# Optimization experiments

Hardware: AMD Instinct MI355X
Metric: run time of the kernel (lower is better)

## Reference

```python
import jax, jax.numpy as jnp
import numpy as np

H = 8  # n_heads

def setup_inputs() -> dict:
    key = jax.random.key(0)
    k1, k2, k3, k4, k5 = jax.random.split(key, 5)
    B, N, D = 4, 2048, 512
    x = jax.random.normal(k1, (B, N, D), dtype=jnp.float32)
    mask_flat = jax.random.randint(k2, (B, N), 0, 2).astype(bool)
    s = 1.0 / np.sqrt(D)
    Wq = jax.random.normal(k3, (D, D), dtype=jnp.float32) * s
    Wkv = jax.random.normal(k4, (D, 2 * D), dtype=jnp.float32) * s
    Wo = jax.random.normal(k5, (D, D), dtype=jnp.float32) * s
    return {"x": x, "mask_flat": mask_flat, "Wq": Wq, "Wkv": Wkv, "Wo": Wo}

def reference(x, mask_flat, Wq, Wkv, Wo):
    B, N, D = x.shape
    d = D // H
    scale = d ** -0.5
    kv = x @ Wkv                                   # (B,N,2D)
    k, v = jnp.split(kv, 2, axis=-1)
    q = x @ Wq                                     # (B,N,D)
    # (B,H,N,d)
    q = q.reshape(B, N, H, d).transpose(0, 2, 1, 3)
    k = k.reshape(B, N, H, d).transpose(0, 2, 1, 3)
    v = v.reshape(B, N, H, d).transpose(0, 2, 1, 3)
    attn = jax.nn.softmax(jnp.einsum('bhmd,bhnd->bhmn', q, k) * scale, axis=-1)
    res = jnp.einsum('bhmn,bhnd->bhmd', attn, v)   # (B,H,N,d)
    out = res.transpose(0, 2, 1, 3).reshape(B, N, D) @ Wo
    # non-masked query positions produce zero output (residual elsewhere keeps them)
    return jnp.where(mask_flat[..., None], out, 0.0)
```

## Files before the change

### kernel.cpp

```cpp
#include <hip/hip_runtime.h>

typedef __bf16 bf16x8 __attribute__((ext_vector_type(8)));
typedef float f32x4 __attribute__((ext_vector_type(4)));
typedef float f32x16 __attribute__((ext_vector_type(16)));
typedef unsigned short u16x8 __attribute__((ext_vector_type(8)));
typedef unsigned int u32x4 __attribute__((ext_vector_type(4)));
typedef int i32x2 __attribute__((ext_vector_type(2)));

__device__ inline unsigned short f2bf(float f) {
    __bf16 h = (__bf16)f;
    return __builtin_bit_cast(unsigned short, h);
}

__device__ inline unsigned int pkbf(float lo, float hi) {
    return (unsigned int)f2bf(lo) | ((unsigned int)f2bf(hi) << 16);
}

__device__ inline float fexp2(float x) {
#if __has_builtin(__builtin_amdgcn_exp2f)
    return __builtin_amdgcn_exp2f(x);
#else
    return exp2f(x);
#endif
}

__device__ inline f32x4 mfma16(u16x8 a, u16x8 b, f32x4 c) {
    return __builtin_amdgcn_mfma_f32_16x16x32_bf16(
        __builtin_bit_cast(bf16x8, a), __builtin_bit_cast(bf16x8, b), c, 0, 0, 0);
}

__device__ inline f32x16 mfma32(u16x8 a, u16x8 b, f32x16 c) {
    return __builtin_amdgcn_mfma_f32_32x32x16_bf16(
        __builtin_bit_cast(bf16x8, a), __builtin_bit_cast(bf16x8, b), c, 0, 0, 0);
}

__device__ inline i32x2 permswap(unsigned int a, unsigned int b, int hi) {
#if __has_builtin(__builtin_amdgcn_permlane32_swap)
    (void)hi;
    return __builtin_amdgcn_permlane32_swap((int)a, (int)b, false, false);
#else
    int pa_ = __shfl_xor((int)a, 32);
    int pb_ = __shfl_xor((int)b, 32);
    i32x2 r;
    r[0] = hi ? pb_ : (int)a;
    r[1] = hi ? (int)b : pa_;
    return r;
#endif
}

__device__ inline void gld_lds16(const unsigned short* gsrc, unsigned short* ldst) {
    __builtin_amdgcn_global_load_lds(
        (const __attribute__((address_space(1))) unsigned int*)gsrc,
        (__attribute__((address_space(3))) unsigned int*)ldst, 16, 0, 0);
}

#define WAIT_VM(n)                                          \
    asm volatile("s_waitcnt vmcnt(" #n ")" ::: "memory");   \
    __builtin_amdgcn_sched_barrier(0)
#define WAIT_LGKM0                                          \
    asm volatile("s_waitcnt lgkmcnt(0)" ::: "memory");      \
    __builtin_amdgcn_sched_barrier(0)
#define BARRIER                                             \
    __builtin_amdgcn_s_barrier();                           \
    __builtin_amdgcn_sched_barrier(0)

__global__ __launch_bounds__(256) void cvt_f32_bf16(const float* __restrict__ in,
                                                    unsigned short* __restrict__ out, long n) {
    long i = ((long)blockIdx.x * blockDim.x + threadIdx.x) * 4;
    if (i >= n) return;
    float4 v = *(const float4*)(in + i);
    ushort4 r;
    r.x = f2bf(v.x); r.y = f2bf(v.y); r.z = f2bf(v.z); r.w = f2bf(v.w);
    *(ushort4*)(out + i) = r;
}

__global__ __launch_bounds__(256) void transpose_cvt_tiled(const float* __restrict__ W,
                                                           unsigned short* __restrict__ Wt,
                                                           int K, int N, float scale) {
    __shared__ float tile[64][65];
    const int n0 = blockIdx.x * 64, k0 = blockIdx.y * 64;
    const int c = threadIdx.x & 63;
    const int r4 = threadIdx.x >> 6;
#pragma unroll
    for (int i = 0; i < 16; i++) {
        int r = r4 * 16 + i;
        tile[r][c] = W[(long)(k0 + r) * N + n0 + c];
    }
    __syncthreads();
#pragma unroll
    for (int i = 0; i < 16; i++) {
        int rr = r4 * 16 + i;
        Wt[(long)(n0 + rr) * K + k0 + c] = f2bf(tile[c][rr] * scale);
    }
}

template<int WRITE_BF16, int MASKED>
__global__ __launch_bounds__(256) void gemm_bt(const unsigned short* __restrict__ A,
                                               const unsigned short* __restrict__ Bt,
                                               void* __restrict__ Cv,
                                               int M, int N, int K,
                                               const int* __restrict__ mask) {
    __shared__ unsigned short AsL[2][128 * 32];
    __shared__ unsigned short BsL[2][128 * 32];
    const int tid = threadIdx.x;
    const int lane = tid & 63;
    const int wid = tid >> 6;
    const int lg = lane >> 4, lr = lane & 15;
    const int wm = wid >> 1, wn = wid & 1;
    const long m0 = (long)blockIdx.y * 128, n0 = (long)blockIdx.x * 128;

    f32x4 acc[4][4] = {};

    const unsigned short* aS0 = A  + (m0 + (tid >> 2)) * K + (tid & 3) * 8;
    const unsigned short* aS1 = A  + (m0 + 64 + (tid >> 2)) * K + (tid & 3) * 8;
    const unsigned short* bS0 = Bt + (n0 + (tid >> 2)) * K + (tid & 3) * 8;
    const unsigned short* bS1 = Bt + (n0 + 64 + (tid >> 2)) * K + (tid & 3) * 8;

#define GSTAGE(bufi, k0v)                                    \
    {                                                        \
        gld_lds16(aS0 + (k0v), &AsL[bufi][wid * 512]);       \
        gld_lds16(aS1 + (k0v), &AsL[bufi][2048 + wid * 512]);\
        gld_lds16(bS0 + (k0v), &BsL[bufi][wid * 512]);       \
        gld_lds16(bS1 + (k0v), &BsL[bufi][2048 + wid * 512]);\
    }

#define GREAD(cur)                                                                    \
    {                                                                                 \
        _Pragma("unroll")                                                             \
        for (int i = 0; i < 4; i++) {                                                 \
            af[i]  = *(const u16x8*)&AsL[cur][(wm * 64 + i * 16 + lr) * 32 + lg * 8]; \
            bfr[i] = *(const u16x8*)&BsL[cur][(wn * 64 + i * 16 + lr) * 32 + lg * 8]; \
        }                                                                             \
    }

#define GMFMA                                                                  \
    {                                                                          \
        _Pragma("unroll")                                                      \
        for (int i = 0; i < 4; i++)                                            \
            _Pragma("unroll")                                                  \
            for (int j = 0; j < 4; j++)                                        \
                acc[i][j] = mfma16(af[i], bfr[j], acc[i][j]);                  \
    }

    const int nk = K >> 5;
    GSTAGE(0, 0);
    GSTAGE(1, 32);
    for (int t = 0; t < nk - 1; t++) {
        const int cur = t & 1;
        u16x8 af[4], bfr[4];
        WAIT_VM(4);
        BARRIER;
        GREAD(cur);
        WAIT_LGKM0;
        BARRIER;
        if (t < nk - 2) GSTAGE(cur, (t + 2) * 32);
        GMFMA;
    }
    {
        u16x8 af[4], bfr[4];
        WAIT_VM(0);
        BARRIER;
        GREAD((nk - 1) & 1);
        GMFMA;
    }
#undef GSTAGE
#undef GREAD
#undef GMFMA

#pragma unroll
    for (int i = 0; i < 4; i++)
#pragma unroll
        for (int j = 0; j < 4; j++)
#pragma unroll
            for (int r = 0; r < 4; r++) {
                long row = m0 + wm * 64 + i * 16 + lg * 4 + r;
                long col = n0 + wn * 64 + j * 16 + lr;
                float v = acc[i][j][r];
                if (MASKED) {
                    if (!mask[row]) v = 0.0f;
                    ((float*)Cv)[row * N + col] = v;
                } else if (WRITE_BF16) {
                    ((unsigned short*)Cv)[row * N + col] = f2bf(v);
                } else {
                    ((float*)Cv)[row * N + col] = v;
                }
            }
}

__global__ __launch_bounds__(256) void attn_kernel(const unsigned short* __restrict__ qk,
                                                   const unsigned short* __restrict__ vT,
                                                   unsigned short* __restrict__ res) {
    const int Nseq = 2048, LD = 1024;
    const long T = 8192;
    const int id = blockIdx.x;
    const int xcd = id & 7, jj = id >> 3;
    const int g = xcd + 8 * (jj & 3);
    const int qt = jj >> 2;
    const int b = g >> 3, h = g & 7;

    const int tid = threadIdx.x;
    const int wid = tid >> 6, lane = tid & 63;
    const int qL = lane & 31, hi = lane >> 5;

    __shared__ unsigned short KsL[2][4096];
    __shared__ unsigned short VsL[2][4096];

    const int qbase = qt * 128 + wid * 32;
    const long qrow = (long)b * Nseq + qbase + qL;
    u16x8 qf[4];
#pragma unroll
    for (int j = 0; j < 4; j++)
        qf[j] = *(const u16x8*)(qk + qrow * LD + h * 64 + 16 * j + 8 * hi);

    f32x16 oacc[2] = {};
    f32x16 lacc = {};
    u16x8 onesf;
#pragma unroll
    for (int e = 0; e < 8; e++) onesf[e] = 0x3F80;

    const int Rsub = lane >> 3, psw = ((lane & 7) ^ (Rsub & 7)) * 8;
    const int R0 = 16 * wid + Rsub;
    const unsigned short* kS = qk + 512 + ((long)b * Nseq + R0) * LD + h * 64 + psw;
    const unsigned short* vS = vT + ((long)h * 64 + R0) * T + (long)b * Nseq + psw;
    const int rsw = qL & 7;

#define STAGE(bufi)                                                            \
    {                                                                          \
        gld_lds16(kS,             &KsL[bufi][(2 * wid + 0) * 512]);            \
        gld_lds16(kS + 8L * LD,   &KsL[bufi][(2 * wid + 1) * 512]);            \
        gld_lds16(vS,             &VsL[bufi][(2 * wid + 0) * 512]);            \
        gld_lds16(vS + 8L * T,    &VsL[bufi][(2 * wid + 1) * 512]);            \
        kS += 64L * LD; vS += 64;                                              \
    }

#define READ_KF(buf)                                                           \
    {                                                                          \
        _Pragma("unroll")                                                      \
        for (int kvb = 0; kvb < 2; kvb++)                                      \
            _Pragma("unroll")                                                  \
            for (int j = 0; j < 4; j++)                                        \
                kf[kvb][j] = *(const u16x8*)&KsL[buf][(kvb * 32 + qL) * 64     \
                                                      + ((2 * j + hi) ^ rsw) * 8]; \
    }
#define READ_VF(buf)                                                           \
    {                                                                          \
        _Pragma("unroll")                                                      \
        for (int db = 0; db < 2; db++)                                         \
            _Pragma("unroll")                                                  \
            for (int jk = 0; jk < 4; jk++)                                     \
                vf[db][jk] = *(const u16x8*)&VsL[buf][(db * 32 + qL) * 64      \
                                                      + ((2 * jk + hi) ^ rsw) * 8]; \
    }

#define PACK_PV(SC)                                                                    \
    {                                                                                  \
        u16x8 pa[4];                                                                   \
        _Pragma("unroll")                                                              \
        for (int kvb = 0; kvb < 2; kvb++) {                                            \
            unsigned int w[8];                                                         \
            _Pragma("unroll")                                                          \
            for (int i = 0; i < 8; i++)                                                \
                w[i] = pkbf(fexp2(SC[kvb][2 * i]), fexp2(SC[kvb][2 * i + 1]));         \
            _Pragma("unroll")                                                          \
            for (int hh = 0; hh < 2; hh++) {                                           \
                i32x2 ra = permswap(w[4 * hh + 0], w[4 * hh + 2], hi);                 \
                i32x2 rb = permswap(w[4 * hh + 1], w[4 * hh + 3], hi);                 \
                u32x4 fw;                                                              \
                fw[0] = (unsigned)ra[0]; fw[1] = (unsigned)rb[0];                      \
                fw[2] = (unsigned)ra[1]; fw[3] = (unsigned)rb[1];                      \
                pa[kvb * 2 + hh] = __builtin_bit_cast(u16x8, fw);                      \
            }                                                                          \
        }                                                                              \
        _Pragma("unroll")                                                              \
        for (int jk = 0; jk < 4; jk++) {                                               \
            lacc = mfma32(pa[jk], onesf, lacc);                                        \
            oacc[0] = mfma32(pa[jk], vf[0][jk], oacc[0]);                              \
            oacc[1] = mfma32(pa[jk], vf[1][jk], oacc[1]);                              \
        }                                                                              \
    }

#define QKNEXT(SN)                                                                     \
    {                                                                                  \
        SN[0] = (f32x16){}; SN[1] = (f32x16){};                                        \
        _Pragma("unroll")                                                              \
        for (int j = 0; j < 4; j++) {                                                  \
            SN[0] = mfma32(kf[0][j], qf[j], SN[0]);                                    \
            SN[1] = mfma32(kf[1][j], qf[j], SN[1]);                                    \
        }                                                                              \
    }

#define STEP(SC, SN, rdbufK, rdbufV, doStage, stagebuf)                                \
    {                                                                                  \
        WAIT_VM(2);                                                                    \
        BARRIER;                                                                       \
        READ_KF(rdbufK);                                                               \
        READ_VF(rdbufV);                                                               \
        WAIT_LGKM0;                                                                    \
        BARRIER;                                                                       \
        if (doStage) STAGE(stagebuf);                                                  \
        QKNEXT(SN);                                                                    \
        PACK_PV(SC);                                                                   \
    }

    u16x8 kf[2][4], vf[2][4];
    f32x16 sA2[2], sB2[2];

    STAGE(0);
    STAGE(1);
    WAIT_VM(6);
    BARRIER;
    READ_KF(0);
    WAIT_LGKM0;
    QKNEXT(sA2);

    for (int t = 0; t < 30; t += 2) {
        STEP(sA2, sB2, 1, 0, 1, 0);
        STEP(sB2, sA2, 0, 1, 1, 1);
    }
    {
        WAIT_VM(2);
        BARRIER;
        READ_KF(1);
        READ_VF(0);
        WAIT_LGKM0;
        QKNEXT(sB2);
        PACK_PV(sA2);
    }
    {
        WAIT_VM(0);
        BARRIER;
        READ_VF(1);
        WAIT_LGKM0;
        PACK_PV(sB2);
    }
#undef STAGE
#undef READ_KF
#undef READ_VF
#undef PACK_PV
#undef QKNEXT
#undef STEP

#pragma unroll
    for (int reg = 0; reg < 16; reg++) {
        const int crow = (reg & 3) + 8 * (reg >> 2) + 4 * hi;
        float linv = 1.0f / lacc[reg];
        long row = (long)b * Nseq + qbase + crow;
        res[row * 512 + h * 64 + qL]      = f2bf(oacc[0][reg] * linv);
        res[row * 512 + h * 64 + 32 + qL] = f2bf(oacc[1][reg] * linv);
    }
}

extern "C" void kernel_launch(void* const* d_in, const int* in_sizes, int n_in,
                              void* d_out, int out_size, void* d_ws, size_t ws_size,
                              hipStream_t stream) {
    const float* x   = (const float*)d_in[0];
    const int* mask  = (const int*)d_in[1];
    const float* Wq  = (const float*)d_in[2];
    const float* Wkv = (const float*)d_in[3];
    const float* Wo  = (const float*)d_in[4];
    float* out = (float*)d_out;

    const int Nseq = 2048, D = 512;
    const long T = 8192;
    const float QSCALE = 0.125f * 1.4426950408889634f;

    unsigned short* ws    = (unsigned short*)d_ws;
    unsigned short* xb    = ws;
    unsigned short* WqkvT = xb    + T * D;
    unsigned short* WoT   = WqkvT + 1536L * 512;
    unsigned short* qkb   = WoT   + 512L * 512;
    unsigned short* vTb   = qkb   + T * 1024;
    unsigned short* resb  = vTb   + 512L * T;

    cvt_f32_bf16<<<(int)(T * D / 1024), 256, 0, stream>>>(x, xb, T * D);
    transpose_cvt_tiled<<<dim3(8, 8),  256, 0, stream>>>(Wq,  WqkvT,              D, 512,  QSCALE);
    transpose_cvt_tiled<<<dim3(16, 8), 256, 0, stream>>>(Wkv, WqkvT + 512L * 512, D, 1024, 1.0f);
    transpose_cvt_tiled<<<dim3(8, 8),  256, 0, stream>>>(Wo,  WoT,                D, 512,  1.0f);

    gemm_bt<1, 0><<<dim3(8, 64), 256, 0, stream>>>(xb, WqkvT, qkb, T, 1024, D, nullptr);
    gemm_bt<1, 0><<<dim3(64, 4), 256, 0, stream>>>(WqkvT + 1024L * 512, xb, vTb, D, T, D, nullptr);

    attn_kernel<<<512, 256, 0, stream>>>(qkb, vTb, resb);

    gemm_bt<0, 1><<<dim3(4, 64), 256, 0, stream>>>(resb, WoT, out, T, D, D, mask);
}
```

Measured before the change: 105.7 us.

## Compact masked query rows to skip attention and output projection work

Adds a per-batch prefix scan over the mask that builds a compacted list of active query indices. The attention kernel then processes only active queries, using 64-query blocks of 128 threads with a deeper staging count, and writes compacted results. The output projection runs on the compacted rows and scatters them to their original positions, while a separate kernel zeroes the masked rows. This removes roughly half the attention and Wo work for a random mask, at the cost of extra launches, gather/scatter indexing and smaller attention blocks.

```diff
diff --git a/kernel.cpp b/kernel.cpp
--- a/kernel.cpp
+++ b/kernel.cpp
@@ -94,12 +94,41 @@
     }
 }
 
-template<int WRITE_BF16, int MASKED>
+__global__ __launch_bounds__(256) void scan_mask(const int* __restrict__ mask,
+                                                 int* __restrict__ idx, int* __restrict__ cnt) {
+    const int b = blockIdx.x;
+    const int tid = threadIdx.x;
+    __shared__ int wsum[4];
+    int m[8]; int pc = 0;
+#pragma unroll
+    for (int k = 0; k < 8; k++) { m[k] = mask[b * 2048 + tid * 8 + k]; pc += (m[k] != 0); }
+    int s = pc;
+    const int lane = tid & 63;
+    for (int off = 1; off < 64; off <<= 1) {
+        int v = __shfl_up(s, off);
+        if (lane >= off) s += v;
+    }
+    if (lane == 63) wsum[tid >> 6] = s;
+    __syncthreads();
+    int wbase = 0;
+    for (int w = 0; w < (tid >> 6); w++) wbase += wsum[w];
+    int run = wbase + s - pc;
+#pragma unroll
+    for (int k = 0; k < 8; k++) if (m[k]) idx[b * 2048 + (run++)] = tid * 8 + k;
+    if (tid == 255) cnt[b] = wbase + s;
+}
+
+__global__ __launch_bounds__(256) void zero_masked(const int* __restrict__ mask,
+                                                   float* __restrict__ out) {
+    long gid = (long)blockIdx.x * 256 + threadIdx.x;
+    int row = (int)(gid >> 7);
+    if (!mask[row]) *(float4*)(out + gid * 4) = make_float4(0.f, 0.f, 0.f, 0.f);
+}
+
 __global__ __launch_bounds__(256) void gemm_bt(const unsigned short* __restrict__ A,
                                                const unsigned short* __restrict__ Bt,
-                                               void* __restrict__ Cv,
-                                               int M, int N, int K,
-                                               const int* __restrict__ mask) {
+                                               unsigned short* __restrict__ C,
+                                               int M, int N, int K) {
     __shared__ unsigned short AsL[2][128 * 32];
     __shared__ unsigned short BsL[2][128 * 32];
     const int tid = threadIdx.x;
@@ -123,7 +152,6 @@
         gld_lds16(bS0 + (k0v), &BsL[bufi][wid * 512]);       \
         gld_lds16(bS1 + (k0v), &BsL[bufi][2048 + wid * 512]);\
     }
-
 #define GREAD(cur)                                                                    \
     {                                                                                 \
         _Pragma("unroll")                                                             \
@@ -132,7 +160,6 @@
             bfr[i] = *(const u16x8*)&BsL[cur][(wn * 64 + i * 16 + lr) * 32 + lg * 8]; \
         }                                                                             \
     }
-
 #define GMFMA                                                                  \
     {                                                                          \
         _Pragma("unroll")                                                      \
@@ -175,21 +202,107 @@
             for (int r = 0; r < 4; r++) {
                 long row = m0 + wm * 64 + i * 16 + lg * 4 + r;
                 long col = n0 + wn * 64 + j * 16 + lr;
-                float v = acc[i][j][r];
-                if (MASKED) {
-                    if (!mask[row]) v = 0.0f;
-                    ((float*)Cv)[row * N + col] = v;
-                } else if (WRITE_BF16) {
-                    ((unsigned short*)Cv)[row * N + col] = f2bf(v);
-                } else {
-                    ((float*)Cv)[row * N + col] = v;
+                C[row * N + col] = f2bf(acc[i][j][r]);
+            }
+}
+
+__global__ __launch_bounds__(256) void gemm_scatter(const unsigned short* __restrict__ A,
+                                                    const unsigned short* __restrict__ Bt,
+                                                    float* __restrict__ out,
+                                                    int N, int K,
+                                                    const int* __restrict__ idxm,
+                                                    const int* __restrict__ cntm) {
+    const long m0 = (long)blockIdx.y * 128;
+    const int bb = (int)(m0 >> 11);
+    const int cnt = cntm[bb];
+    const int i0 = (int)(m0 & 2047);
+    if (i0 >= cnt) return;
+
+    __shared__ unsigned short AsL[2][128 * 32];
+    __shared__ unsigned short BsL[2][128 * 32];
+    const int tid = threadIdx.x;
+    const int lane = tid & 63;
+    const int wid = tid >> 6;
+    const int lg = lane >> 4, lr = lane & 15;
+    const int wm = wid >> 1, wn = wid & 1;
+    const long n0 = (long)blockIdx.x * 128;
+
+    f32x4 acc[4][4] = {};
+
+    const unsigned short* aS0 = A  + (m0 + (tid >> 2)) * K + (tid & 3) * 8;
+    const unsigned short* aS1 = A  + (m0 + 64 + (tid >> 2)) * K + (tid & 3) * 8;
+    const unsigned short* bS0 = Bt + (n0 + (tid >> 2)) * K + (tid & 3) * 8;
+    const unsigned short* bS1 = Bt + (n0 + 64 + (tid >> 2)) * K + (tid & 3) * 8;
+
+#define GSTAGE(bufi, k0v)                                    \
+    {                                                        \
+        gld_lds16(aS0 + (k0v), &AsL[bufi][wid * 512]);       \
+        gld_lds16(aS1 + (k0v), &AsL[bufi][2048 + wid * 512]);\
+        gld_lds16(bS0 + (k0v), &BsL[bufi][wid * 512]);       \
+        gld_lds16(bS1 + (k0v), &BsL[bufi][2048 + wid * 512]);\
+    }
+#define GREAD(cur)                                                                    \
+    {                                                                                 \
+        _Pragma("unroll")                                                             \
+        for (int i = 0; i < 4; i++) {                                                 \
+            af[i]  = *(const u16x8*)&AsL[cur][(wm * 64 + i * 16 + lr) * 32 + lg * 8]; \
+            bfr[i] = *(const u16x8*)&BsL[cur][(wn * 64 + i * 16 + lr) * 32 + lg * 8]; \
+        }                                                                             \
+    }
+#define GMFMA                                                                  \
+    {                                                                          \
+        _Pragma("unroll")                                                      \
+        for (int i = 0; i < 4; i++)                                            \
+            _Pragma("unroll")                                                  \
+            for (int j = 0; j < 4; j++)                                        \
+                acc[i][j] = mfma16(af[i], bfr[j], acc[i][j]);                  \
+    }
+
+    const int nk = K >> 5;
+    GSTAGE(0, 0);
+    GSTAGE(1, 32);
+    for (int t = 0; t < nk - 1; t++) {
+        const int cur = t & 1;
+        u16x8 af[4], bfr[4];
+        WAIT_VM(4);
+        BARRIER;
+        GREAD(cur);
+        WAIT_LGKM0;
+        BARRIER;
+        if (t < nk - 2) GSTAGE(cur, (t + 2) * 32);
+        GMFMA;
+    }
+    {
+        u16x8 af[4], bfr[4];
+        WAIT_VM(0);
+        BARRIER;
+        GREAD((nk - 1) & 1);
+        GMFMA;
+    }
+#undef GSTAGE
+#undef GREAD
+#undef GMFMA
+
+#pragma unroll
+    for (int i = 0; i < 4; i++)
+#pragma unroll
+        for (int j = 0; j < 4; j++)
+#pragma unroll
+            for (int r = 0; r < 4; r++) {
+                int row_c = i0 + wm * 64 + i * 16 + lg * 4 + r;
+                if (row_c < cnt) {
+                    int orig = idxm[bb * 2048 + row_c];
+                    long col = n0 + wn * 64 + j * 16 + lr;
+                    out[((long)bb * 2048 + orig) * N + col] = acc[i][j][r];
                 }
             }
 }
 
-__global__ __launch_bounds__(256) void attn_kernel(const unsigned short* __restrict__ qk,
+__global__ __launch_bounds__(128) void attn_kernel(const unsigned short* __restrict__ qk,
                                                    const unsigned short* __restrict__ vT,
-                                                   unsigned short* __restrict__ res) {
+                                                   unsigned short* __restrict__ res,
+                                                   const int* __restrict__ idxm,
+                                                   const int* __restrict__ cntm) {
     const int Nseq = 2048, LD = 1024;
     const long T = 8192;
     const int id = blockIdx.x;
@@ -198,6 +311,9 @@
     const int qt = jj >> 2;
     const int b = g >> 3, h = g & 7;
 
+    const int count = cntm[b];
+    if (qt * 64 >= count) return;
+
     const int tid = threadIdx.x;
     const int wid = tid >> 6, lane = tid & 63;
     const int qL = lane & 31, hi = lane >> 5;
@@ -205,8 +321,10 @@
     __shared__ unsigned short KsL[2][4096];
     __shared__ unsigned short VsL[2][4096];
 
-    const int qbase = qt * 128 + wid * 32;
-    const long qrow = (long)b * Nseq + qbase + qL;
+    const int qbase = qt * 64 + wid * 32;
+    const int i_q = qbase + qL;
+    const int gi = idxm[b * 2048 + (i_q < count ? i_q : count - 1)];
+    const long qrow = (long)b * Nseq + gi;
     u16x8 qf[4];
 #pragma unroll
     for (int j = 0; j < 4; j++)
@@ -219,17 +337,19 @@
     for (int e = 0; e < 8; e++) onesf[e] = 0x3F80;
 
     const int Rsub = lane >> 3, psw = ((lane & 7) ^ (Rsub & 7)) * 8;
-    const int R0 = 16 * wid + Rsub;
+    const int R0 = 32 * wid + Rsub;
     const unsigned short* kS = qk + 512 + ((long)b * Nseq + R0) * LD + h * 64 + psw;
     const unsigned short* vS = vT + ((long)h * 64 + R0) * T + (long)b * Nseq + psw;
     const int rsw = qL & 7;
 
 #define STAGE(bufi)                                                            \
     {                                                                          \
-        gld_lds16(kS,             &KsL[bufi][(2 * wid + 0) * 512]);            \
-        gld_lds16(kS + 8L * LD,   &KsL[bufi][(2 * wid + 1) * 512]);            \
-        gld_lds16(vS,             &VsL[bufi][(2 * wid + 0) * 512]);            \
-        gld_lds16(vS + 8L * T,    &VsL[bufi][(2 * wid + 1) * 512]);            \
+        _Pragma("unroll")                                                      \
+        for (int i = 0; i < 4; i++)                                            \
+            gld_lds16(kS + (long)i * 8 * LD, &KsL[bufi][(4 * wid + i) * 512]); \
+        _Pragma("unroll")                                                      \
+        for (int i = 0; i < 4; i++)                                            \
+            gld_lds16(vS + (long)i * 8 * T,  &VsL[bufi][(4 * wid + i) * 512]); \
         kS += 64L * LD; vS += 64;                                              \
     }
 
@@ -291,7 +411,7 @@
 
 #define STEP(SC, SN, rdbufK, rdbufV, doStage, stagebuf)                                \
     {                                                                                  \
-        WAIT_VM(2);                                                                    \
+        WAIT_VM(4);                                                                    \
         BARRIER;                                                                       \
         READ_KF(rdbufK);                                                               \
         READ_VF(rdbufV);                                                               \
@@ -307,7 +427,7 @@
 
     STAGE(0);
     STAGE(1);
-    WAIT_VM(6);
+    WAIT_VM(12);
     BARRIER;
     READ_KF(0);
     WAIT_LGKM0;
@@ -318,7 +438,7 @@
         STEP(sB2, sA2, 0, 1, 1, 1);
     }
     {
-        WAIT_VM(2);
+        WAIT_VM(4);
         BARRIER;
         READ_KF(1);
         READ_VF(0);
@@ -343,10 +463,13 @@
 #pragma unroll
     for (int reg = 0; reg < 16; reg++) {
         const int crow = (reg & 3) + 8 * (reg >> 2) + 4 * hi;
-        float linv = 1.0f / lacc[reg];
-        long row = (long)b * Nseq + qbase + crow;
-        res[row * 512 + h * 64 + qL]      = f2bf(oacc[0][reg] * linv);
-        res[row * 512 + h * 64 + 32 + qL] = f2bf(oacc[1][reg] * linv);
+        const int row_c = qbase + crow;
+        if (row_c < count) {
+            float linv = 1.0f / lacc[reg];
+            long row = (long)b * Nseq + row_c;
+            res[row * 512 + h * 64 + qL]      = f2bf(oacc[0][reg] * linv);
+            res[row * 512 + h * 64 + 32 + qL] = f2bf(oacc[1][reg] * linv);
+        }
     }
 }
 
@@ -371,16 +494,20 @@
     unsigned short* qkb   = WoT   + 512L * 512;
     unsigned short* vTb   = qkb   + T * 1024;
     unsigned short* resb  = vTb   + 512L * T;
+    int* idxb = (int*)(resb + T * 512);
+    int* cntb = idxb + 4 * 2048;
 
     cvt_f32_bf16<<<(int)(T * D / 1024), 256, 0, stream>>>(x, xb, T * D);
     transpose_cvt_tiled<<<dim3(8, 8),  256, 0, stream>>>(Wq,  WqkvT,              D, 512,  QSCALE);
     transpose_cvt_tiled<<<dim3(16, 8), 256, 0, stream>>>(Wkv, WqkvT + 512L * 512, D, 1024, 1.0f);
     transpose_cvt_tiled<<<dim3(8, 8),  256, 0, stream>>>(Wo,  WoT,                D, 512,  1.0f);
-
-    gemm_bt<1, 0><<<dim3(8, 64), 256, 0, stream>>>(xb, WqkvT, qkb, T, 1024, D, nullptr);
-    gemm_bt<1, 0><<<dim3(64, 4), 256, 0, stream>>>(WqkvT + 1024L * 512, xb, vTb, D, T, D, nullptr);
-
-    attn_kernel<<<512, 256, 0, stream>>>(qkb, vTb, resb);
-
-    gemm_bt<0, 1><<<dim3(4, 64), 256, 0, stream>>>(resb, WoT, out, T, D, D, mask);
-}
+    scan_mask<<<4, 256, 0, stream>>>(mask, idxb, cntb);
+
+    gemm_bt<<<dim3(8, 64), 256, 0, stream>>>(xb, WqkvT, qkb, T, 1024, D);
+    gemm_bt<<<dim3(64, 4), 256, 0, stream>>>(WqkvT + 1024L * 512, xb, vTb, D, T, D);
+
+    attn_kernel<<<1024, 128, 0, stream>>>(qkb, vTb, resb, idxb, cntb);
+
+    zero_masked<<<(int)(T * 512 / 1024), 256, 0, stream>>>(mask, out);
+    gemm_scatter<<<dim3(4, 64), 256, 0, stream>>>(resb, WoT, out, D, D, idxb, cntb);
+}
```

Measured after the change: 115.8 us. 1.09x slower.

## Compact masked query rows and split KV range across waves in attention

Applied to the files above, without the earlier changes.

Adds a per-batch prefix-scan kernel that compacts the indices of masked-in query positions, so attention runs only over query rows whose output survives the final mask. Each block now handles 64 compacted queries, with the four waves split into two query halves times two KV halves. Each wave stages its own K/V tiles without block barriers, and the partial outputs and row sums are merged through LDS at the end. This roughly halves attention work for a random mask, at the cost of an extra launch, gathered Q loads and scattered result writes. Unmasked rows of res are left unwritten, which is safe only because the output GEMM zeros those rows.

```diff
diff --git a/kernel.cpp b/kernel.cpp
--- a/kernel.cpp
+++ b/kernel.cpp
@@ -92,6 +92,30 @@
         int rr = r4 * 16 + i;
         Wt[(long)(n0 + rr) * K + k0 + c] = f2bf(tile[c][rr] * scale);
     }
+}
+
+__global__ __launch_bounds__(256) void scan_mask(const int* __restrict__ mask,
+                                                 int* __restrict__ idx, int* __restrict__ cnt) {
+    const int b = blockIdx.x;
+    const int tid = threadIdx.x;
+    __shared__ int wsum[4];
+    int m[8]; int pc = 0;
+#pragma unroll
+    for (int k = 0; k < 8; k++) { m[k] = mask[b * 2048 + tid * 8 + k]; pc += (m[k] != 0); }
+    int s = pc;
+    const int lane = tid & 63;
+    for (int off = 1; off < 64; off <<= 1) {
+        int v = __shfl_up(s, off);
+        if (lane >= off) s += v;
+    }
+    if (lane == 63) wsum[tid >> 6] = s;
+    __syncthreads();
+    int wbase = 0;
+    for (int w = 0; w < (tid >> 6); w++) wbase += wsum[w];
+    int run = wbase + s - pc;
+#pragma unroll
+    for (int k = 0; k < 8; k++) if (m[k]) idx[b * 2048 + (run++)] = tid * 8 + k;
+    if (tid == 255) cnt[b] = wbase + s;
 }
 
 template<int WRITE_BF16, int MASKED>
@@ -123,7 +147,6 @@
         gld_lds16(bS0 + (k0v), &BsL[bufi][wid * 512]);       \
         gld_lds16(bS1 + (k0v), &BsL[bufi][2048 + wid * 512]);\
     }
-
 #define GREAD(cur)                                                                    \
     {                                                                                 \
         _Pragma("unroll")                                                             \
@@ -132,7 +155,6 @@
             bfr[i] = *(const u16x8*)&BsL[cur][(wn * 64 + i * 16 + lr) * 32 + lg * 8]; \
         }                                                                             \
     }
-
 #define GMFMA                                                                  \
     {                                                                          \
         _Pragma("unroll")                                                      \
@@ -189,7 +211,9 @@
 
 __global__ __launch_bounds__(256) void attn_kernel(const unsigned short* __restrict__ qk,
                                                    const unsigned short* __restrict__ vT,
-                                                   unsigned short* __restrict__ res) {
+                                                   unsigned short* __restrict__ res,
+                                                   const int* __restrict__ idxm,
+                                                   const int* __restrict__ cntm) {
     const int Nseq = 2048, LD = 1024;
     const long T = 8192;
     const int id = blockIdx.x;
@@ -198,15 +222,20 @@
     const int qt = jj >> 2;
     const int b = g >> 3, h = g & 7;
 
+    const int count = cntm[b];
+    if (qt * 64 >= count) return;
+
     const int tid = threadIdx.x;
     const int wid = tid >> 6, lane = tid & 63;
     const int qL = lane & 31, hi = lane >> 5;
-
-    __shared__ unsigned short KsL[2][4096];
-    __shared__ unsigned short VsL[2][4096];
-
-    const int qbase = qt * 128 + wid * 32;
-    const long qrow = (long)b * Nseq + qbase + qL;
+    const int qh = wid >> 1, kvh = wid & 1;
+
+    __shared__ unsigned short LDSB[4][2][4096];
+    unsigned short* myL = &LDSB[wid][0][0];
+
+    const int i_q = qt * 64 + qh * 32 + qL;
+    const int gi = idxm[b * 2048 + (i_q < count ? i_q : count - 1)];
+    const long qrow = (long)b * Nseq + gi;
     u16x8 qf[4];
 #pragma unroll
     for (int j = 0; j < 4; j++)
@@ -218,135 +247,151 @@
 #pragma unroll
     for (int e = 0; e < 8; e++) onesf[e] = 0x3F80;
 
-    const int Rsub = lane >> 3, psw = ((lane & 7) ^ (Rsub & 7)) * 8;
-    const int R0 = 16 * wid + Rsub;
-    const unsigned short* kS = qk + 512 + ((long)b * Nseq + R0) * LD + h * 64 + psw;
-    const unsigned short* vS = vT + ((long)h * 64 + R0) * T + (long)b * Nseq + psw;
+    const int R0 = lane >> 3, p0 = lane & 7;
+    const unsigned short* kS = qk + 512 + ((long)b * Nseq + kvh * 1024 + R0) * LD + h * 64
+                               + ((p0 ^ R0) * 8);
+    const int rV = lane >> 2, pV = lane & 3;
+    const unsigned short* vS = vT + ((long)h * 64 + rV) * T + (long)b * Nseq + kvh * 1024
+                               + ((pV ^ ((lane >> 3) & 3)) * 8);
     const int rsw = qL & 7;
 
-#define STAGE(bufi)                                                            \
-    {                                                                          \
-        gld_lds16(kS,             &KsL[bufi][(2 * wid + 0) * 512]);            \
-        gld_lds16(kS + 8L * LD,   &KsL[bufi][(2 * wid + 1) * 512]);            \
-        gld_lds16(vS,             &VsL[bufi][(2 * wid + 0) * 512]);            \
-        gld_lds16(vS + 8L * T,    &VsL[bufi][(2 * wid + 1) * 512]);            \
-        kS += 64L * LD; vS += 64;                                              \
+#define STAGE(bufi)                                                          \
+    {                                                                        \
+        unsigned short* dK = myL + (bufi) * 4096;                            \
+        _Pragma("unroll")                                                    \
+        for (int i = 0; i < 4; i++)                                          \
+            gld_lds16(kS + (long)i * 8 * LD, dK + i * 512);                  \
+        _Pragma("unroll")                                                    \
+        for (int i = 0; i < 4; i++)                                          \
+            gld_lds16(vS + (long)i * 16 * T, dK + 2048 + i * 512);           \
+        kS += 32L * LD; vS += 32;                                            \
     }
 
 #define READ_KF(buf)                                                           \
     {                                                                          \
         _Pragma("unroll")                                                      \
-        for (int kvb = 0; kvb < 2; kvb++)                                      \
-            _Pragma("unroll")                                                  \
-            for (int j = 0; j < 4; j++)                                        \
-                kf[kvb][j] = *(const u16x8*)&KsL[buf][(kvb * 32 + qL) * 64     \
-                                                      + ((2 * j + hi) ^ rsw) * 8]; \
+        for (int j = 0; j < 4; j++)                                            \
+            kf[j] = *(const u16x8*)&myL[(buf) * 4096 + qL * 64                 \
+                                        + (((2 * j + hi) ^ rsw) * 8)];         \
     }
 #define READ_VF(buf)                                                           \
     {                                                                          \
         _Pragma("unroll")                                                      \
         for (int db = 0; db < 2; db++)                                         \
             _Pragma("unroll")                                                  \
-            for (int jk = 0; jk < 4; jk++)                                     \
-                vf[db][jk] = *(const u16x8*)&VsL[buf][(db * 32 + qL) * 64      \
-                                                      + ((2 * jk + hi) ^ rsw) * 8]; \
+            for (int jk = 0; jk < 2; jk++)                                     \
+                vf[db][jk] = *(const u16x8*)&myL[(buf) * 4096 + 2048           \
+                                 + (db * 32 + qL) * 32                         \
+                                 + (((2 * jk + hi) ^ ((qL >> 1) & 3)) * 8)];   \
+    }
+
+#define QKNEXT(SN)                                                             \
+    {                                                                          \
+        SN = (f32x16){};                                                       \
+        _Pragma("unroll")                                                      \
+        for (int j = 0; j < 4; j++) SN = mfma32(kf[j], qf[j], SN);             \
     }
 
 #define PACK_PV(SC)                                                                    \
     {                                                                                  \
-        u16x8 pa[4];                                                                   \
+        unsigned int w[8];                                                             \
         _Pragma("unroll")                                                              \
-        for (int kvb = 0; kvb < 2; kvb++) {                                            \
-            unsigned int w[8];                                                         \
-            _Pragma("unroll")                                                          \
-            for (int i = 0; i < 8; i++)                                                \
-                w[i] = pkbf(fexp2(SC[kvb][2 * i]), fexp2(SC[kvb][2 * i + 1]));         \
-            _Pragma("unroll")                                                          \
-            for (int hh = 0; hh < 2; hh++) {                                           \
-                i32x2 ra = permswap(w[4 * hh + 0], w[4 * hh + 2], hi);                 \
-                i32x2 rb = permswap(w[4 * hh + 1], w[4 * hh + 3], hi);                 \
-                u32x4 fw;                                                              \
-                fw[0] = (unsigned)ra[0]; fw[1] = (unsigned)rb[0];                      \
-                fw[2] = (unsigned)ra[1]; fw[3] = (unsigned)rb[1];                      \
-                pa[kvb * 2 + hh] = __builtin_bit_cast(u16x8, fw);                      \
-            }                                                                          \
+        for (int i = 0; i < 8; i++)                                                    \
+            w[i] = pkbf(fexp2(SC[2 * i]), fexp2(SC[2 * i + 1]));                       \
+        u16x8 pa[2];                                                                   \
+        _Pragma("unroll")                                                              \
+        for (int hh = 0; hh < 2; hh++) {                                               \
+            i32x2 ra = permswap(w[4 * hh + 0], w[4 * hh + 2], hi);                     \
+            i32x2 rb = permswap(w[4 * hh + 1], w[4 * hh + 3], hi);                     \
+            u32x4 fw;                                                                  \
+            fw[0] = (unsigned)ra[0]; fw[1] = (unsigned)rb[0];                          \
+            fw[2] = (unsigned)ra[1]; fw[3] = (unsigned)rb[1];                          \
+            pa[hh] = __builtin_bit_cast(u16x8, fw);                                    \
         }                                                                              \
         _Pragma("unroll")                                                              \
-        for (int jk = 0; jk < 4; jk++) {                                               \
+        for (int jk = 0; jk < 2; jk++) {                                               \
             lacc = mfma32(pa[jk], onesf, lacc);                                        \
             oacc[0] = mfma32(pa[jk], vf[0][jk], oacc[0]);                              \
             oacc[1] = mfma32(pa[jk], vf[1][jk], oacc[1]);                              \
         }                                                                              \
     }
 
-#define QKNEXT(SN)                                                                     \
-    {                                                                                  \
-        SN[0] = (f32x16){}; SN[1] = (f32x16){};                                        \
-        _Pragma("unroll")                                                              \
-        for (int j = 0; j < 4; j++) {                                                  \
-            SN[0] = mfma32(kf[0][j], qf[j], SN[0]);                                    \
-            SN[1] = mfma32(kf[1][j], qf[j], SN[1]);                                    \
-        }                                                                              \
-    }
-
-#define STEP(SC, SN, rdbufK, rdbufV, doStage, stagebuf)                                \
-    {                                                                                  \
-        WAIT_VM(2);                                                                    \
-        BARRIER;                                                                       \
-        READ_KF(rdbufK);                                                               \
-        READ_VF(rdbufV);                                                               \
-        WAIT_LGKM0;                                                                    \
-        BARRIER;                                                                       \
-        if (doStage) STAGE(stagebuf);                                                  \
-        QKNEXT(SN);                                                                    \
-        PACK_PV(SC);                                                                   \
-    }
-
-    u16x8 kf[2][4], vf[2][4];
-    f32x16 sA2[2], sB2[2];
+#define STEP(SC, SN, cur)                                                      \
+    {                                                                          \
+        WAIT_VM(4);                                                            \
+        READ_VF(cur);                                                          \
+        READ_KF(cur ^ 1);                                                      \
+        WAIT_LGKM0;                                                            \
+        STAGE(cur);                                                            \
+        QKNEXT(SN);                                                            \
+        PACK_PV(SC);                                                           \
+    }
+
+    u16x8 kf[4], vf[2][2];
+    f32x16 sA, sB;
 
     STAGE(0);
     STAGE(1);
-    WAIT_VM(6);
-    BARRIER;
+    WAIT_VM(12);
     READ_KF(0);
     WAIT_LGKM0;
-    QKNEXT(sA2);
+    QKNEXT(sA);
 
     for (int t = 0; t < 30; t += 2) {
-        STEP(sA2, sB2, 1, 0, 1, 0);
-        STEP(sB2, sA2, 0, 1, 1, 1);
+        STEP(sA, sB, 0);
+        STEP(sB, sA, 1);
     }
     {
-        WAIT_VM(2);
-        BARRIER;
+        WAIT_VM(4);
+        READ_VF(0);
         READ_KF(1);
-        READ_VF(0);
         WAIT_LGKM0;
-        QKNEXT(sB2);
-        PACK_PV(sA2);
+        QKNEXT(sB);
+        PACK_PV(sA);
     }
     {
         WAIT_VM(0);
-        BARRIER;
         READ_VF(1);
         WAIT_LGKM0;
-        PACK_PV(sB2);
+        PACK_PV(sB);
     }
 #undef STAGE
 #undef READ_KF
 #undef READ_VF
+#undef QKNEXT
 #undef PACK_PV
-#undef QKNEXT
 #undef STEP
 
-#pragma unroll
-    for (int reg = 0; reg < 16; reg++) {
-        const int crow = (reg & 3) + 8 * (reg >> 2) + 4 * hi;
-        float linv = 1.0f / lacc[reg];
-        long row = (long)b * Nseq + qbase + crow;
-        res[row * 512 + h * 64 + qL]      = f2bf(oacc[0][reg] * linv);
-        res[row * 512 + h * 64 + 32 + qL] = f2bf(oacc[1][reg] * linv);
+    __syncthreads();
+    float* Ox = (float*)&LDSB[0][0][0];
+    float* lX = Ox + 2 * 32 * 65;
+
+    if (kvh == 1) {
+#pragma unroll
+        for (int reg = 0; reg < 16; reg++) {
+            const int crow = (reg & 3) + 8 * (reg >> 2) + 4 * hi;
+            Ox[qh * 2080 + crow * 65 + qL]      = oacc[0][reg];
+            Ox[qh * 2080 + crow * 65 + 32 + qL] = oacc[1][reg];
+            lX[qh * 32 + crow] = lacc[reg];
+        }
+    }
+    __syncthreads();
+    if (kvh == 0) {
+#pragma unroll
+        for (int reg = 0; reg < 16; reg++) {
+            const int crow = (reg & 3) + 8 * (reg >> 2) + 4 * hi;
+            const int row_c = qt * 64 + qh * 32 + crow;
+            if (row_c < count) {
+                float lt = lacc[reg] + lX[qh * 32 + crow];
+                float linv = 1.0f / lt;
+                float o0 = oacc[0][reg] + Ox[qh * 2080 + crow * 65 + qL];
+                float o1 = oacc[1][reg] + Ox[qh * 2080 + crow * 65 + 32 + qL];
+                const int orig = idxm[b * 2048 + row_c];
+                long row = (long)b * Nseq + orig;
+                res[row * 512 + h * 64 + qL]      = f2bf(o0 * linv);
+                res[row * 512 + h * 64 + 32 + qL] = f2bf(o1 * linv);
+            }
+        }
     }
 }
 
@@ -371,16 +416,19 @@
     unsigned short* qkb   = WoT   + 512L * 512;
     unsigned short* vTb   = qkb   + T * 1024;
     unsigned short* resb  = vTb   + 512L * T;
+    int* idxb = (int*)(resb + T * 512);
+    int* cntb = idxb + 4 * 2048;
 
     cvt_f32_bf16<<<(int)(T * D / 1024), 256, 0, stream>>>(x, xb, T * D);
     transpose_cvt_tiled<<<dim3(8, 8),  256, 0, stream>>>(Wq,  WqkvT,              D, 512,  QSCALE);
     transpose_cvt_tiled<<<dim3(16, 8), 256, 0, stream>>>(Wkv, WqkvT + 512L * 512, D, 1024, 1.0f);
     transpose_cvt_tiled<<<dim3(8, 8),  256, 0, stream>>>(Wo,  WoT,                D, 512,  1.0f);
+    scan_mask<<<4, 256, 0, stream>>>(mask, idxb, cntb);
 
     gemm_bt<1, 0><<<dim3(8, 64), 256, 0, stream>>>(xb, WqkvT, qkb, T, 1024, D, nullptr);
     gemm_bt<1, 0><<<dim3(64, 4), 256, 0, stream>>>(WqkvT + 1024L * 512, xb, vTb, D, T, D, nullptr);
 
-    attn_kernel<<<512, 256, 0, stream>>>(qkb, vTb, resb);
+    attn_kernel<<<1024, 256, 0, stream>>>(qkb, vTb, resb, idxb, cntb);
 
     gemm_bt<0, 1><<<dim3(4, 64), 256, 0, stream>>>(resb, WoT, out, T, D, D, mask);
 }
```

Result: no change. 107.4 us (+1.6%).
